# Performance work log

Measured on AMD Instinct MI355X. Metric: run time of the kernel, lower is better.

## Reference

```python
import jax, jax.numpy as jnp
import numpy as np

B, N, D = 4, 300, 256
G, PIN, POUT = 4, 32, 128
CG = D // G
TOTAL = CG * CG + PIN * POUT
STRIDES = (8, 16, 32, 64)
SIZES = ((100, 160), (50, 80), (25, 40), (13, 20))
TAU = 2.0
MAP_STRIDE = 3.0  # log2(stride of level 0) = log2(8)


def setup_inputs():
    key = jax.random.key(0)
    ks = jax.random.split(key, 16)
    inp = {}
    for i, (h, w) in enumerate(SIZES):
        inp['feat%d' % i] = jax.random.normal(ks[i], (B, D, h, w), jnp.float32)
    inp['query_feat'] = jax.random.normal(ks[4], (B, N, D), jnp.float32)
    xy = jax.random.uniform(ks[5], (B, N, 2), jnp.float32) * jnp.array([1280.0, 800.0], jnp.float32)
    z = jax.random.uniform(ks[6], (B, N, 1), jnp.float32) * 2.0 + 4.0
    r = jax.random.normal(ks[7], (B, N, 1), jnp.float32) * 0.3
    inp['query_roi'] = jnp.concatenate([xy, z, r], axis=-1)
    inp['off_w'] = jax.random.normal(ks[8], (D, G * PIN * 3), jnp.float32) * 0.01
    bias = jnp.concatenate([jax.random.uniform(ks[9], (G, PIN, 2), jnp.float32, -0.5, 0.5),
                            jnp.full((G, PIN, 1), -1.0, jnp.float32)], axis=-1)
    inp['off_b'] = bias.reshape(-1)
    inp['pg_w'] = jax.random.normal(ks[10], (D, G * TOTAL), jnp.float32) * 0.02
    inp['pg_b'] = jnp.zeros((G * TOTAL,), jnp.float32)
    inp['op_w'] = jax.random.normal(ks[11], (G * POUT * CG, D), jnp.float32) * 0.01
    inp['op_b'] = jnp.zeros((D,), jnp.float32)
    inp['ln_g'] = jnp.ones((D,), jnp.float32)
    inp['ln_b'] = jnp.zeros((D,), jnp.float32)
    return inp


def _ln2(x, eps=1e-5):
    # F.layer_norm over last two dims, no affine
    mu = jnp.mean(x, axis=(-2, -1), keepdims=True)
    var = jnp.mean((x - mu) ** 2, axis=(-2, -1), keepdims=True)
    return (x - mu) * jax.lax.rsqrt(var + eps)


def _ln1(x, eps=1e-5):
    mu = jnp.mean(x, axis=-1, keepdims=True)
    var = jnp.mean((x - mu) ** 2, axis=-1, keepdims=True)
    return (x - mu) * jax.lax.rsqrt(var + eps)


def _bilinear(feat, px, py, w):
    # feat [B,D,H,W]; px,py,w [B,N,G,PIN] (pixel coords, grid_sample align_corners=False, zero pad)
    H, W = feat.shape[2], feat.shape[3]
    v = feat.reshape(B, G, CG, H * W).transpose(0, 1, 3, 2)  # [B,G,HW,CG]
    x0 = jnp.floor(px)
    y0 = jnp.floor(py)
    wx1 = px - x0
    wy1 = py - y0

    def corner(xf, yf, cw):
        xi = xf.astype(jnp.int32)
        yi = yf.astype(jnp.int32)
        valid = (xi >= 0) & (xi < W) & (yi >= 0) & (yi < H)
        idx = jnp.clip(yi, 0, H - 1) * W + jnp.clip(xi, 0, W - 1)       # [B,N,G,PIN]
        idx = idx.transpose(0, 2, 1, 3).reshape(B, G, N * PIN, 1)
        g = jnp.take_along_axis(v, idx, axis=2)                          # [B,G,N*PIN,CG]
        g = g.reshape(B, G, N, PIN, CG).transpose(0, 2, 1, 3, 4)
        return g * (cw * valid.astype(cw.dtype))[..., None]

    acc = (corner(x0, y0, (1 - wx1) * (1 - wy1)) + corner(x0 + 1, y0, wx1 * (1 - wy1)) +
           corner(x0, y0 + 1, (1 - wx1) * wy1) + corner(x0 + 1, y0 + 1, wx1 * wy1))
    return acc * w[..., None]


def _forward(feats, query_feat, query_roi, off_w, off_b, pg_w, pg_b, op_w, op_b, ln_g, ln_b):
    # make_sample_points
    offset = (query_feat @ off_w + off_b).reshape(B, N, G * PIN, 3)
    roi_cc = query_roi[..., :2]
    scale = 2.0 ** query_roi[..., 2:3]
    ratio = 2.0 ** jnp.concatenate([query_roi[..., 3:4] * -0.5, query_roi[..., 3:4] * 0.5], axis=-1)
    roi_wh = scale * ratio                                               # [B,N,2]
    sample_xy = roi_cc[:, :, None, :] + offset[..., :2] * roi_wh[:, :, None, :]  # [B,N,G*PIN,2]
    sample_z = query_roi[..., 2:3] + offset[..., 2]                      # [B,N,G*PIN]
    # level weights: softmax over levels of -(z-3-l)^2/tau
    lvl = jnp.arange(len(STRIDES), dtype=sample_z.dtype)
    lw = jax.nn.softmax(-((sample_z - MAP_STRIDE)[..., None] - lvl) ** 2 / TAU, axis=-1)
    sx = sample_xy[..., 0].reshape(B, N, G, PIN)
    sy = sample_xy[..., 1].reshape(B, N, G, PIN)
    sampled = jnp.zeros((B, N, G, PIN, CG), query_feat.dtype)
    for li, (feat, stride) in enumerate(zip(feats, STRIDES)):
        wl = lw[..., li].reshape(B, N, G, PIN)
        sampled = sampled + _bilinear(feat, sx / stride - 0.5, sy / stride - 0.5, wl)
    # AdaptiveMixing
    params = (query_feat @ pg_w + pg_b).reshape(B, N, G, TOTAL)
    M = params[..., :CG * CG].reshape(B, N, G, CG, CG)
    S = params[..., CG * CG:].reshape(B, N, G, POUT, PIN)
    h = jnp.einsum('bngpc,bngcd->bngpd', sampled, M)
    h = jax.nn.relu(_ln2(h))
    h = jnp.einsum('bngop,bngpd->bngod', S, h)
    h = jax.nn.relu(_ln2(h))
    h = query_feat + (h.reshape(B, N, G * POUT * CG) @ op_w + op_b)
    return _ln1(h) * ln_g + ln_b


def reference(feat0, feat1, feat2, feat3, query_feat, query_roi, off_w, off_b, pg_w, pg_b, op_w, op_b, ln_g, ln_b):
    return _forward([feat0, feat1, feat2, feat3], query_feat, query_roi,
                    off_w, off_b, pg_w, pg_b, op_w, op_b, ln_g, ln_b)
```

## Files before the change

kernel.cpp:

```cpp
#include <hip/hip_runtime.h>
#include <hip/hip_bf16.h>
#include <cstdint>

namespace {

constexpr int B = 4, N = 300, D = 256;
constexpr int G = 4, PIN = 32, POUT = 128;
constexpr int CG = D / G;
constexpr int TOTAL = CG * CG + PIN * POUT;
constexpr int BN_TOT = B * N;
constexpr int BN_PAD = 1216;
constexpr int GT = G * TOTAL;

typedef short s16x8 __attribute__((ext_vector_type(8)));
typedef float f32x4 __attribute__((ext_vector_type(4)));

__device__ __forceinline__ float bf2f(unsigned short u) {
  union { unsigned int i; float f; } x; x.i = ((unsigned int)u) << 16; return x.f;
}
__device__ __forceinline__ unsigned short f2bf(float f) {
  union { float f; unsigned int i; } x; x.f = f;
  unsigned int r = x.i + 0x7fffu + ((x.i >> 16) & 1u);
  return (unsigned short)(r >> 16);
}

__device__ __forceinline__ void breduce2(float& a, float& b, volatile float* red) {
  __syncthreads();
  #pragma unroll
  for (int off = 32; off; off >>= 1) {
    a += __shfl_down(a, off, 64);
    b += __shfl_down(b, off, 64);
  }
  int t = threadIdx.x;
  if ((t & 63) == 0) { red[t >> 6] = a; red[4 + (t >> 6)] = b; }
  __syncthreads();
  a = red[0] + red[1] + red[2] + red[3];
  b = red[4] + red[5] + red[6] + red[7];
}

__global__ __launch_bounds__(256) void k_transpose(
    const float* __restrict__ in, unsigned short* __restrict__ out, int R, int C) {
  __shared__ unsigned short T[64][72];
  int c0 = blockIdx.x * 64;
  int r0 = blockIdx.y * 64;
  int t = threadIdx.x;
  #pragma unroll
  for (int i = 0; i < 4; ++i) {
    int u = t + i * 256;
    int rr = u >> 4, c4 = (u & 15) * 4;
    float4 v = *(const float4*)(in + (size_t)(r0 + rr) * C + c0 + c4);
    ushort4 w;
    w.x = f2bf(v.x); w.y = f2bf(v.y); w.z = f2bf(v.z); w.w = f2bf(v.w);
    *(ushort4*)&T[rr][c4] = w;
  }
  __syncthreads();
  #pragma unroll
  for (int i = 0; i < 2; ++i) {
    int u = t + i * 256;
    int c = u >> 3, rr8 = (u & 7) * 8;
    unsigned short tmp[8];
    #pragma unroll
    for (int j = 0; j < 8; ++j) tmp[j] = T[rr8 + j][c];
    *(uint4*)(out + (size_t)(c0 + c) * R + r0 + rr8) = *(const uint4*)tmp;
  }
}

__global__ __launch_bounds__(256) void k_featT(
    const float* __restrict__ in, unsigned short* __restrict__ out, int HW) {
  __shared__ unsigned short T[64][72];
  int hw0 = blockIdx.x * 64;
  int d0 = blockIdx.y * 64;
  int bb = blockIdx.z;
  int t = threadIdx.x;
  #pragma unroll
  for (int i = 0; i < 4; ++i) {
    int u = t + i * 256;
    int rr = u >> 4, c4 = (u & 15) * 4;
    if (hw0 + c4 + 3 < HW) {
      float4 v = *(const float4*)(in + ((size_t)(bb * D + d0 + rr)) * HW + hw0 + c4);
      ushort4 w;
      w.x = f2bf(v.x); w.y = f2bf(v.y); w.z = f2bf(v.z); w.w = f2bf(v.w);
      *(ushort4*)&T[rr][c4] = w;
    }
  }
  __syncthreads();
  #pragma unroll
  for (int i = 0; i < 2; ++i) {
    int u = t + i * 256;
    int p = u >> 3, dd8 = (u & 7) * 8;
    if (hw0 + p < HW) {
      unsigned short tmp[8];
      #pragma unroll
      for (int j = 0; j < 8; ++j) tmp[j] = T[dd8 + j][p];
      *(uint4*)(out + ((size_t)(bb * HW + hw0 + p)) * D + d0 + dd8) = *(const uint4*)tmp;
    }
  }
}

__global__ __launch_bounds__(256) void k_cvt_qf(
    const float* __restrict__ qf, unsigned short* __restrict__ qb) {
  int e = (blockIdx.x * 256 + threadIdx.x) * 4;
  int row = e >> 8;
  ushort4 w;
  if (row < BN_TOT) {
    float4 v = *(const float4*)(qf + e);
    w.x = f2bf(v.x); w.y = f2bf(v.y); w.z = f2bf(v.z); w.w = f2bf(v.w);
  } else {
    w.x = w.y = w.z = w.w = 0;
  }
  *(ushort4*)(qb + e) = w;
}

__global__ __launch_bounds__(384) void k_off(
    const float* __restrict__ qf, const float* __restrict__ offw,
    const float* __restrict__ offb, float* __restrict__ offsets) {
  int r0 = blockIdx.x * 16;
  int t = threadIdx.x;
  __shared__ float Q[16][256];
  for (int i = t; i < 16 * 256; i += 384)
    Q[i >> 8][i & 255] = qf[(size_t)(r0 + (i >> 8)) * 256 + (i & 255)];
  __syncthreads();
  float acc[16];
  float bias = offb[t];
  #pragma unroll
  for (int r = 0; r < 16; ++r) acc[r] = bias;
  for (int d = 0; d < 256; ++d) {
    float w = offw[(size_t)d * 384 + t];
    #pragma unroll
    for (int r = 0; r < 16; ++r) acc[r] += Q[r][d] * w;
  }
  #pragma unroll
  for (int r = 0; r < 16; ++r) offsets[(size_t)(r0 + r) * 384 + t] = acc[r];
}

__global__ __launch_bounds__(256) void k_gather(
    const float* __restrict__ roi, const float* __restrict__ offsets,
    const unsigned short* __restrict__ featT, unsigned short* __restrict__ sampled) {
  int bn = blockIdx.x;
  int bb = bn / N;
  int t = threadIdx.x;
  __shared__ int   widx[2048];
  __shared__ float wval[2048];

  const int Wl[4] = {160, 80, 40, 20};
  const int Hl[4] = {100, 50, 25, 13};
  const int loff[4] = {0, 16384000, 20480000, 21504000};
  const int HWl[4] = {16000, 4000, 1000, 260};
  const float sl[4] = {8.f, 16.f, 32.f, 64.f};

  float cx = roi[bn * 4 + 0], cy = roi[bn * 4 + 1];
  float z = roi[bn * 4 + 2], r = roi[bn * 4 + 3];
  float scale = exp2f(z);
  float rwx = scale * exp2f(-0.5f * r);
  float rhy = scale * exp2f(0.5f * r);

  #pragma unroll
  for (int task = t; task < 512; task += 256) {
    int j = task >> 2, l = task & 3;
    float ox = offsets[(size_t)bn * 384 + j * 3 + 0];
    float oy = offsets[(size_t)bn * 384 + j * 3 + 1];
    float oz = offsets[(size_t)bn * 384 + j * 3 + 2];
    float sx = cx + ox * rwx;
    float sy = cy + oy * rhy;
    float sz = z + oz;
    float lw[4];
    float m = -1e30f;
    #pragma unroll
    for (int ll = 0; ll < 4; ++ll) {
      float dlt = sz - 3.0f - (float)ll;
      lw[ll] = -dlt * dlt * 0.5f;
      m = fmaxf(m, lw[ll]);
    }
    float s = 0.f;
    #pragma unroll
    for (int ll = 0; ll < 4; ++ll) { lw[ll] = expf(lw[ll] - m); s += lw[ll]; }
    float wl_ = lw[l] / s;

    int W = Wl[l], H = Hl[l];
    float px = sx / sl[l] - 0.5f;
    float py = sy / sl[l] - 0.5f;
    float x0f = floorf(px), y0f = floorf(py);
    int x0 = (int)x0f, y0 = (int)y0f;
    float fx = px - x0f, fy = py - y0f;
    int base = loff[l] + bb * HWl[l] * 256;
    #pragma unroll
    for (int k = 0; k < 4; ++k) {
      int xi = x0 + (k & 1), yi = y0 + (k >> 1);
      bool valid = (xi >= 0) & (xi < W) & (yi >= 0) & (yi < H);
      int xc = min(max(xi, 0), W - 1), yc = min(max(yi, 0), H - 1);
      float wgt = ((k & 1) ? fx : 1.f - fx) * ((k >> 1) ? fy : 1.f - fy) * wl_;
      widx[j * 16 + l * 4 + k] = base + (yc * W + xc) * 256;
      wval[j * 16 + l * 4 + k] = valid ? wgt : 0.f;
    }
  }
  __syncthreads();

  int wave = t >> 6, lane = t & 63;
  int half = lane >> 5, ln = lane & 31;
  const unsigned short* fb = featT + wave * 64 + ln * 2;
  #pragma unroll 2
  for (int it = 0; it < 16; ++it) {
    int p = it * 2 + half;
    int j = wave * 32 + p;
    int ix[16]; float w[16]; unsigned int u[16];
    #pragma unroll
    for (int k = 0; k < 16; ++k) { ix[k] = widx[j * 16 + k]; w[k] = wval[j * 16 + k]; }
    #pragma unroll
    for (int k = 0; k < 16; ++k) u[k] = *(const unsigned int*)(fb + ix[k]);
    float a0 = 0.f, a1 = 0.f;
    #pragma unroll
    for (int k = 0; k < 16; ++k) {
      a0 += w[k] * bf2f((unsigned short)(u[k] & 0xffffu));
      a1 += w[k] * bf2f((unsigned short)(u[k] >> 16));
    }
    unsigned int packed = (unsigned int)f2bf(a0) | ((unsigned int)f2bf(a1) << 16);
    *(unsigned int*)(sampled + (((size_t)bn * G + wave) * PIN + p) * CG + ln * 2) = packed;
  }
}

__global__ __launch_bounds__(256) void k_pgemm(
    const unsigned short* __restrict__ A, const unsigned short* __restrict__ Bt,
    const float* __restrict__ pgb, unsigned short* __restrict__ params) {
  __shared__ unsigned short As[64][72];
  __shared__ unsigned short Bs[128][72];
  int col0 = blockIdx.x * 128;
  int row0 = blockIdx.y * 64;
  int t = threadIdx.x;
  int wave = t >> 6, lane = t & 63, lr = lane & 15, q = lane >> 4;
  f32x4 acc[4][2] = {};
  for (int k0 = 0; k0 < D; k0 += 64) {
    #pragma unroll
    for (int i = 0; i < 2; ++i) {
      int u = t + i * 256;
      int r = u >> 3, kk = (u & 7) * 8;
      *(uint4*)&As[r][kk] = *(const uint4*)(A + (size_t)(row0 + r) * D + k0 + kk);
    }
    #pragma unroll
    for (int i = 0; i < 4; ++i) {
      int u = t + i * 256;
      int n = u >> 3, kk = (u & 7) * 8;
      *(uint4*)&Bs[n][kk] = *(const uint4*)(Bt + (size_t)(col0 + n) * D + k0 + kk);
    }
    __syncthreads();
    #pragma unroll
    for (int ks = 0; ks < 64; ks += 32) {
      s16x8 af[4], bf[2];
      #pragma unroll
      for (int mi = 0; mi < 4; ++mi)
        af[mi] = *(const s16x8*)&As[mi * 16 + lr][ks + q * 8];
      #pragma unroll
      for (int ni = 0; ni < 2; ++ni)
        bf[ni] = *(const s16x8*)&Bs[wave * 32 + ni * 16 + lr][ks + q * 8];
      #pragma unroll
      for (int mi = 0; mi < 4; ++mi)
        #pragma unroll
        for (int ni = 0; ni < 2; ++ni)
          acc[mi][ni] = __builtin_amdgcn_mfma_f32_16x16x32_bf16(af[mi], bf[ni], acc[mi][ni], 0, 0, 0);
    }
    __syncthreads();
  }
  #pragma unroll
  for (int ni = 0; ni < 2; ++ni) {
    int c = col0 + wave * 32 + ni * 16 + lr;
    float bias = pgb[c];
    #pragma unroll
    for (int mi = 0; mi < 4; ++mi) {
      #pragma unroll
      for (int rg = 0; rg < 4; ++rg) {
        int rr = row0 + mi * 16 + q * 4 + rg;
        if (rr < BN_TOT) params[(size_t)rr * GT + c] = f2bf(acc[mi][ni][rg] + bias);
      }
    }
  }
}

__global__ __launch_bounds__(256) void k_mixing(
    const unsigned short* __restrict__ sampled, const unsigned short* __restrict__ params,
    unsigned short* __restrict__ h2out) {
  int blk = blockIdx.x;
  int g = blk & 3;
  int bn = blk >> 2;
  const unsigned short* P = params + ((size_t)bn * GT) + (size_t)g * TOTAL;
  __shared__ float Sam[PIN * CG];
  __shared__ float Ms[CG * CG];
  __shared__ float H1[PIN * CG];
  __shared__ float red[8];
  int t = threadIdx.x;
  const unsigned short* sp = sampled + (((size_t)bn * G + g) * PIN) * CG;
  for (int i = t; i < PIN * CG; i += 256) Sam[i] = bf2f(sp[i]);
  for (int i = t; i < CG * CG; i += 256) Ms[i] = bf2f(P[i]);
  __syncthreads();

  int p = t >> 3, db = (t & 7) * 8;
  float h[8] = {};
  for (int c = 0; c < CG; ++c) {
    float s = Sam[p * CG + c];
    #pragma unroll
    for (int i = 0; i < 8; ++i) h[i] += s * Ms[c * CG + db + i];
  }
  float a = 0.f, b2 = 0.f;
  #pragma unroll
  for (int i = 0; i < 8; ++i) { a += h[i]; b2 += h[i] * h[i]; }
  breduce2(a, b2, red);
  {
    float mu = a * (1.f / (PIN * CG));
    float var = b2 * (1.f / (PIN * CG)) - mu * mu;
    float rs = rsqrtf(var + 1e-5f);
    #pragma unroll
    for (int i = 0; i < 8; ++i) {
      float v = (h[i] - mu) * rs;
      H1[p * CG + db + i] = v > 0.f ? v : 0.f;
    }
  }
  __syncthreads();

  int o = t >> 1, d2 = (t & 1) * 32;
  float h2r[32] = {};
  for (int pp = 0; pp < PIN; ++pp) {
    float sv = bf2f(P[CG * CG + o * PIN + pp]);
    #pragma unroll
    for (int i = 0; i < 32; ++i) h2r[i] += sv * H1[pp * CG + d2 + i];
  }
  a = 0.f; b2 = 0.f;
  #pragma unroll
  for (int i = 0; i < 32; ++i) { a += h2r[i]; b2 += h2r[i] * h2r[i]; }
  breduce2(a, b2, red);
  {
    float mu = a * (1.f / (POUT * CG));
    float var = b2 * (1.f / (POUT * CG)) - mu * mu;
    float rs = rsqrtf(var + 1e-5f);
    unsigned short* dst = h2out + (size_t)bn * GT + (size_t)g * TOTAL + o * CG + d2;
    #pragma unroll
    for (int i = 0; i < 32; ++i) {
      float v = (h2r[i] - mu) * rs;
      dst[i] = f2bf(v > 0.f ? v : 0.f);
    }
  }
}

constexpr int KSPLIT = 32, KCH = GT / KSPLIT;
__global__ __launch_bounds__(256) void k_ogemm(
    const unsigned short* __restrict__ A, const unsigned short* __restrict__ Bt,
    float* __restrict__ parts) {
  __shared__ unsigned short As[64][72];
  __shared__ unsigned short Bs[256][72];
  int row0 = blockIdx.x * 64;
  int z = blockIdx.y;
  int kbase = z * KCH;
  int t = threadIdx.x;
  int wave = t >> 6, lane = t & 63, lr = lane & 15, q = lane >> 4;
  f32x4 acc[4][4] = {};
  for (int k0 = 0; k0 < KCH; k0 += 64) {
    #pragma unroll
    for (int i = 0; i < 2; ++i) {
      int u = t + i * 256;
      int r = u >> 3, kk = (u & 7) * 8;
      *(uint4*)&As[r][kk] = *(const uint4*)(A + (size_t)(row0 + r) * GT + kbase + k0 + kk);
    }
    #pragma unroll
    for (int i = 0; i < 8; ++i) {
      int u = t + i * 256;
      int n = u >> 3, kk = (u & 7) * 8;
      *(uint4*)&Bs[n][kk] = *(const uint4*)(Bt + (size_t)n * GT + kbase + k0 + kk);
    }
    __syncthreads();
    #pragma unroll
    for (int ks = 0; ks < 64; ks += 32) {
      s16x8 af[4], bf[4];
      #pragma unroll
      for (int mi = 0; mi < 4; ++mi)
        af[mi] = *(const s16x8*)&As[mi * 16 + lr][ks + q * 8];
      #pragma unroll
      for (int ni = 0; ni < 4; ++ni)
        bf[ni] = *(const s16x8*)&Bs[wave * 64 + ni * 16 + lr][ks + q * 8];
      #pragma unroll
      for (int mi = 0; mi < 4; ++mi)
        #pragma unroll
        for (int ni = 0; ni < 4; ++ni)
          acc[mi][ni] = __builtin_amdgcn_mfma_f32_16x16x32_bf16(af[mi], bf[ni], acc[mi][ni], 0, 0, 0);
    }
    __syncthreads();
  }
  #pragma unroll
  for (int mi = 0; mi < 4; ++mi) {
    #pragma unroll
    for (int ni = 0; ni < 4; ++ni) {
      int c = wave * 64 + ni * 16 + lr;
      #pragma unroll
      for (int rg = 0; rg < 4; ++rg) {
        int rr = row0 + mi * 16 + q * 4 + rg;
        if (rr < BN_TOT)
          parts[((size_t)z * BN_PAD + rr) * D + c] = acc[mi][ni][rg];
      }
    }
  }
}

__global__ __launch_bounds__(256) void k_final(
    const float* __restrict__ qf, const float* __restrict__ opb,
    const float* __restrict__ parts, const float* __restrict__ lng,
    const float* __restrict__ lnb, float* __restrict__ out) {
  int bn = blockIdx.x;
  int d = threadIdx.x;
  float v = qf[(size_t)bn * D + d] + opb[d];
  #pragma unroll
  for (int s = 0; s < KSPLIT; ++s) v += parts[((size_t)s * BN_PAD + bn) * D + d];
  __shared__ float red[8];
  float a = v, b2 = v * v;
  breduce2(a, b2, red);
  float mu = a * (1.f / D);
  float var = b2 * (1.f / D) - mu * mu;
  float rs = rsqrtf(var + 1e-5f);
  out[(size_t)bn * D + d] = (v - mu) * rs * lng[d] + lnb[d];
}

}

extern "C" void kernel_launch(void* const* d_in, const int* in_sizes, int n_in,
                              void* d_out, int out_size, void* d_ws, size_t ws_size,
                              hipStream_t stream) {
  const float* f0 = (const float*)d_in[0];
  const float* f1 = (const float*)d_in[1];
  const float* f2 = (const float*)d_in[2];
  const float* f3 = (const float*)d_in[3];
  const float* qf = (const float*)d_in[4];
  const float* roi = (const float*)d_in[5];
  const float* off_w = (const float*)d_in[6];
  const float* off_b = (const float*)d_in[7];
  const float* pg_w = (const float*)d_in[8];
  const float* pg_b = (const float*)d_in[9];
  const float* op_w = (const float*)d_in[10];
  const float* op_b = (const float*)d_in[11];
  const float* ln_g = (const float*)d_in[12];
  const float* ln_b = (const float*)d_in[13];
  float* out = (float*)d_out;

  char* ws = (char*)d_ws;
  unsigned short* sampled = (unsigned short*)ws;
  unsigned short* h2      = (unsigned short*)(ws + 19660800ULL);
  unsigned short* featT   = h2;
  unsigned short* params  = (unsigned short*)(ws + 19660800ULL + 79691776ULL);
  float*          parts   = (float*)(ws + 19660800ULL + 79691776ULL);
  unsigned short* wT      = (unsigned short*)(ws + 19660800ULL + 2 * 79691776ULL);
  unsigned short* qfb     = (unsigned short*)(ws + 19660800ULL + 2 * 79691776ULL + 16777216ULL);
  float*          offsets = (float*)(ws + 19660800ULL + 2 * 79691776ULL + 16777216ULL + 622592ULL);

  k_featT<<<dim3(250, 4, B), 256, 0, stream>>>(f0, featT + 0,        16000);
  k_featT<<<dim3( 63, 4, B), 256, 0, stream>>>(f1, featT + 16384000, 4000);
  k_featT<<<dim3( 16, 4, B), 256, 0, stream>>>(f2, featT + 20480000, 1000);
  k_featT<<<dim3(  5, 4, B), 256, 0, stream>>>(f3, featT + 21504000, 260);
  k_off<<<BN_TOT / 16, 384, 0, stream>>>(qf, off_w, off_b, offsets);
  k_transpose<<<dim3(GT / 64, D / 64), 256, 0, stream>>>(pg_w, wT, D, GT);
  k_cvt_qf<<<BN_PAD * D / 1024, 256, 0, stream>>>(qf, qfb);
  k_gather<<<BN_TOT, 256, 0, stream>>>(roi, offsets, featT, sampled);
  k_pgemm<<<dim3(GT / 128, BN_PAD / 64), 256, 0, stream>>>(qfb, wT, pg_b, params);
  k_mixing<<<BN_TOT * G, 256, 0, stream>>>(sampled, params, h2);
  k_transpose<<<dim3(D / 64, GT / 64), 256, 0, stream>>>(op_w, wT, GT, D);
  k_ogemm<<<dim3(BN_PAD / 64, KSPLIT), 256, 0, stream>>>(h2, wT, parts);
  k_final<<<BN_TOT, 256, 0, stream>>>(qf, op_b, parts, ln_g, ln_b, out);
}
```

Baseline: 482.2 us.

## Use MFMA for adaptive mixing matmuls with transposed M layout from param GEMM

The per-query mixing kernel's two small matmuls move from scalar FP32 loops over shared memory to bf16 MFMA instructions that read operands straight from global memory. The first matmul needs M in transposed form, so the weight transpose feeding the parameter GEMM permutes the M columns and the bias lookup is remapped to match. This cuts shared-memory traffic and scalar FMA work in the mixing stage. In exchange the intermediate activation is rounded to bf16, and the output stores become strided scalar writes.

```diff
diff --git a/kernel.cpp b/kernel.cpp
--- a/kernel.cpp
+++ b/kernel.cpp
@@ -39,7 +39,8 @@
 }
 
 __global__ __launch_bounds__(256) void k_transpose(
-    const float* __restrict__ in, unsigned short* __restrict__ out, int R, int C) {
+    const float* __restrict__ in, unsigned short* __restrict__ out, int R, int C,
+    int mperm) {
   __shared__ unsigned short T[64][72];
   int c0 = blockIdx.x * 64;
   int r0 = blockIdx.y * 64;
@@ -61,7 +62,12 @@
     unsigned short tmp[8];
     #pragma unroll
     for (int j = 0; j < 8; ++j) tmp[j] = T[rr8 + j][c];
-    *(uint4*)(out + (size_t)(c0 + c) * R + r0 + rr8) = *(const uint4*)tmp;
+    int n = c0 + c;
+    if (mperm) {
+      int local = n & 8191;
+      if (local < 4096) n = (n & ~8191) | ((local & 63) << 6) | (local >> 6);
+    }
+    *(uint4*)(out + (size_t)n * R + r0 + rr8) = *(const uint4*)tmp;
   }
 }
 
@@ -262,7 +268,9 @@
   #pragma unroll
   for (int ni = 0; ni < 2; ++ni) {
     int c = col0 + wave * 32 + ni * 16 + lr;
-    float bias = pgb[c];
+    int local = c & 8191;
+    int cb = (local < 4096) ? ((c & ~8191) | ((local & 63) << 6) | (local >> 6)) : c;
+    float bias = pgb[cb];
     #pragma unroll
     for (int mi = 0; mi < 4; ++mi) {
       #pragma unroll
@@ -275,65 +283,87 @@
 }
 
 __global__ __launch_bounds__(256) void k_mixing(
-    const unsigned short* __restrict__ sampled, const unsigned short* __restrict__ params,
+    const unsigned short* __restrict__ sampled,
+    const unsigned short* __restrict__ params,
     unsigned short* __restrict__ h2out) {
   int blk = blockIdx.x;
-  int g = blk & 3;
-  int bn = blk >> 2;
-  const unsigned short* P = params + ((size_t)bn * GT) + (size_t)g * TOTAL;
-  __shared__ float Sam[PIN * CG];
-  __shared__ float Ms[CG * CG];
-  __shared__ float H1[PIN * CG];
+  int g = blk & 3, bn = blk >> 2;
+  const unsigned short* P = params + (size_t)bn * GT + (size_t)g * TOTAL;
+  const unsigned short* Sp = sampled + (((size_t)bn * G + g) * PIN) * CG;
+  __shared__ unsigned short Ht[64][40];
   __shared__ float red[8];
   int t = threadIdx.x;
-  const unsigned short* sp = sampled + (((size_t)bn * G + g) * PIN) * CG;
-  for (int i = t; i < PIN * CG; i += 256) Sam[i] = bf2f(sp[i]);
-  for (int i = t; i < CG * CG; i += 256) Ms[i] = bf2f(P[i]);
-  __syncthreads();
-
-  int p = t >> 3, db = (t & 7) * 8;
-  float h[8] = {};
-  for (int c = 0; c < CG; ++c) {
-    float s = Sam[p * CG + c];
-    #pragma unroll
-    for (int i = 0; i < 8; ++i) h[i] += s * Ms[c * CG + db + i];
-  }
-  float a = 0.f, b2 = 0.f;
-  #pragma unroll
-  for (int i = 0; i < 8; ++i) { a += h[i]; b2 += h[i] * h[i]; }
-  breduce2(a, b2, red);
+  int w = t >> 6, lane = t & 63, lr = lane & 15, q = lane >> 4;
+
+  f32x4 acc1[2] = {};
+  #pragma unroll
+  for (int ks = 0; ks < 2; ++ks) {
+    s16x8 b = *(const s16x8*)(P + (w * 16 + lr) * 64 + ks * 32 + q * 8);
+    #pragma unroll
+    for (int mt = 0; mt < 2; ++mt) {
+      s16x8 a = *(const s16x8*)(Sp + (mt * 16 + lr) * 64 + ks * 32 + q * 8);
+      acc1[mt] = __builtin_amdgcn_mfma_f32_16x16x32_bf16(a, b, acc1[mt], 0, 0, 0);
+    }
+  }
+  float s1 = 0.f, ss1 = 0.f;
+  #pragma unroll
+  for (int mt = 0; mt < 2; ++mt)
+    #pragma unroll
+    for (int rg = 0; rg < 4; ++rg) { float v = acc1[mt][rg]; s1 += v; ss1 += v * v; }
+  breduce2(s1, ss1, red);
   {
-    float mu = a * (1.f / (PIN * CG));
-    float var = b2 * (1.f / (PIN * CG)) - mu * mu;
+    float mu = s1 * (1.f / 2048.f);
+    float var = ss1 * (1.f / 2048.f) - mu * mu;
     float rs = rsqrtf(var + 1e-5f);
     #pragma unroll
-    for (int i = 0; i < 8; ++i) {
-      float v = (h[i] - mu) * rs;
-      H1[p * CG + db + i] = v > 0.f ? v : 0.f;
-    }
-  }
-  __syncthreads();
-
-  int o = t >> 1, d2 = (t & 1) * 32;
-  float h2r[32] = {};
-  for (int pp = 0; pp < PIN; ++pp) {
-    float sv = bf2f(P[CG * CG + o * PIN + pp]);
-    #pragma unroll
-    for (int i = 0; i < 32; ++i) h2r[i] += sv * H1[pp * CG + d2 + i];
-  }
-  a = 0.f; b2 = 0.f;
-  #pragma unroll
-  for (int i = 0; i < 32; ++i) { a += h2r[i]; b2 += h2r[i] * h2r[i]; }
-  breduce2(a, b2, red);
+    for (int mt = 0; mt < 2; ++mt) {
+      unsigned short pk[4];
+      #pragma unroll
+      for (int rg = 0; rg < 4; ++rg) {
+        float v = (acc1[mt][rg] - mu) * rs;
+        pk[rg] = f2bf(v > 0.f ? v : 0.f);
+      }
+      *(uint2*)&Ht[w * 16 + lr][mt * 16 + q * 4] = *(const uint2*)pk;
+    }
+  }
+  __syncthreads();
+
+  f32x4 acc2[2][4] = {};
+  #pragma unroll
+  for (int mt = 0; mt < 2; ++mt) {
+    int o = w * 32 + mt * 16 + lr;
+    s16x8 a = *(const s16x8*)(P + 4096 + o * 32 + q * 8);
+    #pragma unroll
+    for (int nt = 0; nt < 4; ++nt) {
+      s16x8 b = *(const s16x8*)&Ht[nt * 16 + lr][q * 8];
+      acc2[mt][nt] = __builtin_amdgcn_mfma_f32_16x16x32_bf16(a, b, acc2[mt][nt], 0, 0, 0);
+    }
+  }
+  float s2 = 0.f, ss2 = 0.f;
+  #pragma unroll
+  for (int mt = 0; mt < 2; ++mt)
+    #pragma unroll
+    for (int nt = 0; nt < 4; ++nt)
+      #pragma unroll
+      for (int rg = 0; rg < 4; ++rg) { float v = acc2[mt][nt][rg]; s2 += v; ss2 += v * v; }
+  breduce2(s2, ss2, red);
   {
-    float mu = a * (1.f / (POUT * CG));
-    float var = b2 * (1.f / (POUT * CG)) - mu * mu;
+    float mu = s2 * (1.f / 8192.f);
+    float var = ss2 * (1.f / 8192.f) - mu * mu;
     float rs = rsqrtf(var + 1e-5f);
-    unsigned short* dst = h2out + (size_t)bn * GT + (size_t)g * TOTAL + o * CG + d2;
-    #pragma unroll
-    for (int i = 0; i < 32; ++i) {
-      float v = (h2r[i] - mu) * rs;
-      dst[i] = f2bf(v > 0.f ? v : 0.f);
+    unsigned short* dst = h2out + (size_t)bn * GT + (size_t)g * TOTAL;
+    #pragma unroll
+    for (int mt = 0; mt < 2; ++mt) {
+      #pragma unroll
+      for (int nt = 0; nt < 4; ++nt) {
+        int d = nt * 16 + lr;
+        #pragma unroll
+        for (int rg = 0; rg < 4; ++rg) {
+          int o = w * 32 + mt * 16 + q * 4 + rg;
+          float v = (acc2[mt][nt][rg] - mu) * rs;
+          dst[o * 64 + d] = f2bf(v > 0.f ? v : 0.f);
+        }
+      }
     }
   }
 }
@@ -450,12 +480,12 @@
   k_featT<<<dim3( 16, 4, B), 256, 0, stream>>>(f2, featT + 20480000, 1000);
   k_featT<<<dim3(  5, 4, B), 256, 0, stream>>>(f3, featT + 21504000, 260);
   k_off<<<BN_TOT / 16, 384, 0, stream>>>(qf, off_w, off_b, offsets);
-  k_transpose<<<dim3(GT / 64, D / 64), 256, 0, stream>>>(pg_w, wT, D, GT);
+  k_transpose<<<dim3(GT / 64, D / 64), 256, 0, stream>>>(pg_w, wT, D, GT, 1);
   k_cvt_qf<<<BN_PAD * D / 1024, 256, 0, stream>>>(qf, qfb);
   k_gather<<<BN_TOT, 256, 0, stream>>>(roi, offsets, featT, sampled);
   k_pgemm<<<dim3(GT / 128, BN_PAD / 64), 256, 0, stream>>>(qfb, wT, pg_b, params);
   k_mixing<<<BN_TOT * G, 256, 0, stream>>>(sampled, params, h2);
-  k_transpose<<<dim3(D / 64, GT / 64), 256, 0, stream>>>(op_w, wT, GT, D);
+  k_transpose<<<dim3(D / 64, GT / 64), 256, 0, stream>>>(op_w, wT, GT, D, 0);
   k_ogemm<<<dim3(BN_PAD / 64, KSPLIT), 256, 0, stream>>>(h2, wT, parts);
   k_final<<<BN_TOT, 256, 0, stream>>>(qf, op_b, parts, ln_g, ln_b, out);
 }
```

After: 421.1 us. 12.7% less time.
